# Optimization experiments

Hardware: AMD Instinct MI355X
Metric: run time of the kernel (lower is better)

## Reference

```python
import jax, jax.numpy as jnp
import numpy as np

NUM_NODES = 100000
NUM_EDGES = 50000
N_INC = 1000000  # incidence pairs (node, hyperedge)
IN_DIM = 128
EDGE_DIM = 128
NODE_DIM = 128


def _glorot(key, fan_in, fan_out):
    lim = float(np.sqrt(6.0 / (fan_in + fan_out)))
    return jax.random.uniform(key, (fan_in, fan_out), jnp.float32, -lim, lim)


def _prelu(x, a):
    return jnp.where(x >= 0, x, a * x)


def setup_inputs() -> dict:
    key = jax.random.key(0)
    ks = jax.random.split(key, 7)
    x = jax.random.normal(ks[0], (NUM_NODES, IN_DIM), jnp.float32)
    node_idx = jax.random.randint(ks[1], (N_INC,), 0, NUM_NODES, jnp.int32)
    edge_idx = jax.random.randint(ks[2], (N_INC,), 0, NUM_EDGES, jnp.int32)
    hyperedge_index = jnp.stack([node_idx, edge_idx])  # [2, N_INC]
    return dict(
        x=x,
        hyperedge_index=hyperedge_index,
        W_n2e_0=_glorot(ks[3], IN_DIM, EDGE_DIM),
        W_e2n_0=_glorot(ks[4], EDGE_DIM, NODE_DIM),
        bias_0=jnp.zeros((NODE_DIM,), jnp.float32),
        W_n2e_1=_glorot(ks[5], NODE_DIM, EDGE_DIM),
        W_e2n_1=_glorot(ks[6], EDGE_DIM, NODE_DIM),
        bias_1=jnp.zeros((NODE_DIM,), jnp.float32),
        alpha=jnp.float32(0.25),  # shared nn.PReLU() parameter
        num_nodes=NUM_NODES,
        num_edges=NUM_EDGES,
    )


def _conv(x, node_idx, edge_idx, Dn_inv, De_inv, W_n2e, W_e2n, b, alpha,
          num_nodes, num_edges):
    # node -> hyperedge: row-normalized scatter-add (norm = De^{-1} per target edge)
    xe = x @ W_n2e                                              # [N, E_dim]
    msg_e = xe[node_idx] * De_inv[edge_idx][:, None]            # [N_INC, E_dim]
    e = jax.ops.segment_sum(msg_e, edge_idx, num_segments=num_edges)
    e = _prelu(e, alpha)
    # hyperedge -> node: norm = Dn^{-1} per target node
    xn = e @ W_e2n                                              # [M, D]
    msg_n = xn[edge_idx] * Dn_inv[node_idx][:, None]            # [N_INC, D]
    n = jax.ops.segment_sum(msg_n, node_idx, num_segments=num_nodes) + b
    return n, e


def reference(x, hyperedge_index, W_n2e_0, W_e2n_0, bias_0, W_n2e_1, W_e2n_1,
              bias_1, alpha, num_nodes, num_edges):
    node_idx = hyperedge_index[0]
    edge_idx = hyperedge_index[1]
    ones = jnp.ones((node_idx.shape[0],), jnp.float32)
    Dn = jax.ops.segment_sum(ones, node_idx, num_segments=num_nodes)
    De = jax.ops.segment_sum(ones, edge_idx, num_segments=num_edges)
    Dn_inv = jnp.where(Dn > 0, 1.0 / jnp.where(Dn > 0, Dn, 1.0), 0.0)
    De_inv = jnp.where(De > 0, 1.0 / jnp.where(De > 0, De, 1.0), 0.0)

    n, e = _conv(x, node_idx, edge_idx, Dn_inv, De_inv,
                 W_n2e_0, W_e2n_0, bias_0, alpha, num_nodes, num_edges)
    n = _prelu(n, alpha)  # encoder-level activation between layers
    n, e = _conv(n, node_idx, edge_idx, Dn_inv, De_inv,
                 W_n2e_1, W_e2n_1, bias_1, alpha, num_nodes, num_edges)
    n = _prelu(n, alpha)
    return n, e
```

## Files before the change

### kernel.cpp

```cpp
#include <hip/hip_runtime.h>
#include <stdint.h>

#define NN 100000
#define NE 50000
#define NBLK 256
#define NBK 196
#define ESH 8
#define NSH 9

using bf16x8 = __attribute__((ext_vector_type(8))) short;
using f32x4  = __attribute__((ext_vector_type(4))) float;

__device__ inline unsigned f2bf(float f) {
  union { float f; unsigned u; } x; x.f = f;
  unsigned u = x.u;
  return (u + 0x7FFFu + ((u >> 16) & 1u)) >> 16;
}
__device__ inline float bfbits2f(unsigned bits) {
  union { unsigned u; float f; } x; x.u = bits;
  return x.f;
}


__global__ __launch_bounds__(256) void hist_kernel(const int* __restrict__ nidx,
                                                   const int* __restrict__ eidx, int ni,
                                                   int* __restrict__ He, int* __restrict__ Hn) {
  __shared__ int he[NBK], hn[NBK];
  for (int t = threadIdx.x; t < NBK; t += 256) { he[t] = 0; hn[t] = 0; }
  __syncthreads();
  int chunk = (ni + NBLK - 1) / NBLK;
  int s = blockIdx.x * chunk, e = min(s + chunk, ni);
  for (int i = s + threadIdx.x; i < e; i += 256) {
    atomicAdd(&he[eidx[i] >> ESH], 1);
    atomicAdd(&hn[nidx[i] >> NSH], 1);
  }
  __syncthreads();
  for (int t = threadIdx.x; t < NBK; t += 256) {
    He[t * NBLK + blockIdx.x] = he[t];
    Hn[t * NBLK + blockIdx.x] = hn[t];
  }
}

__global__ __launch_bounds__(256) void scanH_kernel(int* __restrict__ He, int* __restrict__ Hn,
                                                    int* __restrict__ ebb, int* __restrict__ nbb,
                                                    int ni) {
  int* H = blockIdx.x ? Hn : He;
  int* bb = blockIdx.x ? nbb : ebb;
  __shared__ int tot[256];
  int t = threadIdx.x;
  int sum = 0;
  if (t < NBK)
    for (int b = 0; b < NBLK; b++) sum += H[t * NBLK + b];
  tot[t] = sum;
  __syncthreads();
  for (int o = 1; o < 256; o <<= 1) {
    int v = (t >= o) ? tot[t - o] : 0;
    __syncthreads();
    tot[t] += v;
    __syncthreads();
  }
  int base = (t > 0) ? tot[t - 1] : 0;
  if (t < NBK) {
    bb[t] = base;
    int run = base;
    for (int b = 0; b < NBLK; b++) {
      int old = H[t * NBLK + b];
      H[t * NBLK + b] = run;
      run += old;
    }
  }
  if (t == 0) bb[NBK] = ni;
}

__global__ __launch_bounds__(256) void scatter_kernel(const int* __restrict__ nidx,
                                                      const int* __restrict__ eidx, int ni,
                                                      const int* __restrict__ He,
                                                      const int* __restrict__ Hn,
                                                      unsigned* __restrict__ binE,
                                                      unsigned* __restrict__ binN) {
  __shared__ int ce[NBK], cn[NBK];
  for (int t = threadIdx.x; t < NBK; t += 256) {
    ce[t] = He[t * NBLK + blockIdx.x];
    cn[t] = Hn[t * NBLK + blockIdx.x];
  }
  __syncthreads();
  int chunk = (ni + NBLK - 1) / NBLK;
  int s = blockIdx.x * chunk, e = min(s + chunk, ni);
  for (int i = s + threadIdx.x; i < e; i += 256) {
    int nd = nidx[i], ed = eidx[i];
    int pe = atomicAdd(&ce[ed >> ESH], 1);
    binE[pe] = (unsigned)nd | ((unsigned)(ed & 255) << 17);
    int pn = atomicAdd(&cn[nd >> NSH], 1);
    binN[pn] = (unsigned)ed | ((unsigned)(nd & 511) << 16);
  }
}

__global__ __launch_bounds__(256) void finalize_kernel(const unsigned* __restrict__ binE,
                                                       const unsigned* __restrict__ binN,
                                                       const int* __restrict__ ebb,
                                                       const int* __restrict__ nbb,
                                                       int* __restrict__ eoff, int* __restrict__ noff,
                                                       float* __restrict__ einv, float* __restrict__ ninv,
                                                       int* __restrict__ edge_nodes,
                                                       int* __restrict__ node_edges, int ni) {
  __shared__ int cnt[512], excl[512], sc[256];
  bool isE = blockIdx.x < NBK;
  int b = isE ? blockIdx.x : blockIdx.x - NBK;
  const unsigned* bin = isE ? binE : binN;
  const int* bb = isE ? ebb : nbb;
  int* off = isE ? eoff : noff;
  float* inv = isE ? einv : ninv;
  int* out = isE ? edge_nodes : node_edges;
  int NT = isE ? NE : NN;
  int sh = isE ? ESH : NSH;
  int psh = isE ? 17 : 16;
  unsigned smask = (1u << psh) - 1u;
  int tbase = b << sh;
  int nt = min(1 << sh, NT - tbase);
  int t = threadIdx.x;
  cnt[t] = 0; cnt[t + 256] = 0;
  __syncthreads();
  int s = bb[b], e = bb[b + 1];
  for (int i = s + t; i < e; i += 256) atomicAdd(&cnt[bin[i] >> psh], 1);
  __syncthreads();
  int p = cnt[2 * t] + cnt[2 * t + 1];
  sc[t] = p;
  __syncthreads();
  for (int o = 1; o < 256; o <<= 1) {
    int v = (t >= o) ? sc[t - o] : 0;
    __syncthreads();
    sc[t] += v;
    __syncthreads();
  }
  int pb = (t > 0) ? sc[t - 1] : 0;
  excl[2 * t] = pb;
  excl[2 * t + 1] = pb + cnt[2 * t];
  __syncthreads();
  for (int lt = t; lt < nt; lt += 256) {
    off[tbase + lt] = s + excl[lt];
    int c = cnt[lt];
    inv[tbase + lt] = (c > 0) ? 1.0f / (float)c : 0.0f;
  }
  if (b == NBK - 1 && t == 0) off[NT] = ni;
  __syncthreads();
  cnt[t] = 0; cnt[t + 256] = 0;
  __syncthreads();
  for (int i = s + t; i < e; i += 256) {
    unsigned it = bin[i];
    int lt = it >> psh;
    int pos = s + excl[lt] + atomicAdd(&cnt[lt], 1);
    out[pos] = (int)(it & smask);
  }
}

__global__ void packw_kernel(const float* __restrict__ w0, const float* __restrict__ w1,
                             const float* __restrict__ w2, const float* __restrict__ w3,
                             short* __restrict__ wp) {
  int gid = blockIdx.x * blockDim.x + threadIdx.x;
  if (gid >= 4 * 16384) return;
  int w = gid >> 14, r = gid & 16383;
  int j = r & 7, lane = (r >> 3) & 63, kk = (r >> 9) & 3, ct = (r >> 11) & 7;
  int k = kk * 32 + (lane >> 4) * 8 + j;
  int c = ct * 16 + (lane & 15);
  const float* W = (w == 0) ? w0 : (w == 1) ? w1 : (w == 2) ? w2 : w3;
  wp[gid] = (short)f2bf(W[k * 128 + c]);
}

__global__ __launch_bounds__(256) void cvtrow_kernel(const float* __restrict__ x,
                                                     uint4* __restrict__ xb) {
  size_t q = (size_t)blockIdx.x * 256 + threadIdx.x;
  const float4* xf = (const float4*)x;
  float4 lo = xf[q * 2], hi = xf[q * 2 + 1];
  uint4 o;
  o.x = (f2bf(lo.x) & 0xffffu) | (f2bf(lo.y) << 16);
  o.y = (f2bf(lo.z) & 0xffffu) | (f2bf(lo.w) << 16);
  o.z = (f2bf(hi.x) & 0xffffu) | (f2bf(hi.y) << 16);
  o.w = (f2bf(hi.z) & 0xffffu) | (f2bf(hi.w) << 16);
  xb[q] = o;
}

template <bool PRELU, bool OBF>
__global__ __launch_bounds__(256) void gather_kernel(const uint4* __restrict__ src,
                                                     void* __restrict__ dst,
                                                     const int* __restrict__ off,
                                                     const int* __restrict__ ids,
                                                     const float* __restrict__ inv,
                                                     const float* __restrict__ bias,
                                                     const float* __restrict__ alpha_p, int T) {
  int tgt = blockIdx.x * 16 + (threadIdx.x >> 4);
  if (tgt >= T) return;
  int c = threadIdx.x & 15;
  int s = off[tgt], e = off[tgt + 1];
  float r[8] = {0, 0, 0, 0, 0, 0, 0, 0};
  int i = s;
  for (; i + 8 <= e; i += 8) {
    int idv[8];
#pragma unroll
    for (int u = 0; u < 8; u++) idv[u] = ids[i + u];
    uint4 v[8];
#pragma unroll
    for (int u = 0; u < 8; u++) v[u] = src[(size_t)idv[u] * 16 + c];
#pragma unroll
    for (int u = 0; u < 8; u++) {
      r[0] += bfbits2f(v[u].x << 16); r[1] += bfbits2f(v[u].x & 0xffff0000u);
      r[2] += bfbits2f(v[u].y << 16); r[3] += bfbits2f(v[u].y & 0xffff0000u);
      r[4] += bfbits2f(v[u].z << 16); r[5] += bfbits2f(v[u].z & 0xffff0000u);
      r[6] += bfbits2f(v[u].w << 16); r[7] += bfbits2f(v[u].w & 0xffff0000u);
    }
  }
  for (; i < e; i++) {
    uint4 v = src[(size_t)ids[i] * 16 + c];
    r[0] += bfbits2f(v.x << 16); r[1] += bfbits2f(v.x & 0xffff0000u);
    r[2] += bfbits2f(v.y << 16); r[3] += bfbits2f(v.y & 0xffff0000u);
    r[4] += bfbits2f(v.z << 16); r[5] += bfbits2f(v.z & 0xffff0000u);
    r[6] += bfbits2f(v.w << 16); r[7] += bfbits2f(v.w & 0xffff0000u);
  }
  float scv = inv[tgt];
  float al = PRELU ? *alpha_p : 0.f;
  float b[8] = {0, 0, 0, 0, 0, 0, 0, 0};
  if (bias) {
    float4 b0 = ((const float4*)bias)[c * 2];
    float4 b1 = ((const float4*)bias)[c * 2 + 1];
    b[0] = b0.x; b[1] = b0.y; b[2] = b0.z; b[3] = b0.w;
    b[4] = b1.x; b[5] = b1.y; b[6] = b1.z; b[7] = b1.w;
  }
#pragma unroll
  for (int j = 0; j < 8; j++) {
    float v = r[j] * scv + b[j];
    if constexpr (PRELU) v = (v >= 0.f) ? v : al * v;
    r[j] = v;
  }
  if constexpr (OBF) {
    uint4 o;
    o.x = (f2bf(r[0]) & 0xffffu) | (f2bf(r[1]) << 16);
    o.y = (f2bf(r[2]) & 0xffffu) | (f2bf(r[3]) << 16);
    o.z = (f2bf(r[4]) & 0xffffu) | (f2bf(r[5]) << 16);
    o.w = (f2bf(r[6]) & 0xffffu) | (f2bf(r[7]) << 16);
    ((uint4*)dst)[(size_t)tgt * 16 + c] = o;
  } else {
    float4 o0; o0.x = r[0]; o0.y = r[1]; o0.z = r[2]; o0.w = r[3];
    float4 o1; o1.x = r[4]; o1.y = r[5]; o1.z = r[6]; o1.w = r[7];
    ((float4*)dst)[(size_t)tgt * 32 + c * 2] = o0;
    ((float4*)dst)[(size_t)tgt * 32 + c * 2 + 1] = o1;
  }
}

template <bool WEF32>
__global__ __launch_bounds__(256) void gemm12_kernel(const short* __restrict__ A,
                                                     const short* __restrict__ wpA,
                                                     const short* __restrict__ wpB,
                                                     const float* __restrict__ alpha_p,
                                                     short* __restrict__ xn,
                                                     float* __restrict__ eoutf, int M) {
  __shared__ short tile[64][136];
  int wave = threadIdx.x >> 6;
  int lane = threadIdx.x & 63;
  int kg = lane >> 4;
  int rloc = lane & 15;
  int base = blockIdx.x * 64;
  int row = base + wave * 16 + rloc;
  float al = *alpha_p;

  bf16x8 a[4];
  if (row < M) {
    const short* arow = A + (size_t)row * 128 + kg * 8;
#pragma unroll
    for (int kk = 0; kk < 4; kk++) a[kk] = *(const bf16x8*)(arow + kk * 32);
  } else {
#pragma unroll
    for (int kk = 0; kk < 4; kk++) a[kk] = bf16x8{0, 0, 0, 0, 0, 0, 0, 0};
  }

#pragma unroll
  for (int ct = 0; ct < 8; ct++) {
    f32x4 acc = {0.f, 0.f, 0.f, 0.f};
#pragma unroll
    for (int kk = 0; kk < 4; kk++) {
      bf16x8 bfr = *(const bf16x8*)(wpA + ((size_t)(ct * 4 + kk) * 64 + lane) * 8);
      acc = __builtin_amdgcn_mfma_f32_16x16x32_bf16(a[kk], bfr, acc, 0, 0, 0);
    }
    int col = ct * 16 + rloc;
#pragma unroll
    for (int j = 0; j < 4; j++) {
      float v = acc[j];
      v = (v >= 0.f) ? v : al * v;
      int lrow = wave * 16 + kg * 4 + j;
      int grow = base + lrow;
      if (WEF32 && grow < M) eoutf[(size_t)grow * 128 + col] = v;
      tile[lrow][col] = (short)f2bf(v);
    }
  }

  bf16x8 a2[4];
#pragma unroll
  for (int kk = 0; kk < 4; kk++)
    a2[kk] = *(const bf16x8*)&tile[wave * 16 + rloc][kg * 8 + kk * 32];
#pragma unroll
  for (int ct = 0; ct < 8; ct++) {
    f32x4 acc = {0.f, 0.f, 0.f, 0.f};
#pragma unroll
    for (int kk = 0; kk < 4; kk++) {
      bf16x8 bfr = *(const bf16x8*)(wpB + ((size_t)(ct * 4 + kk) * 64 + lane) * 8);
      acc = __builtin_amdgcn_mfma_f32_16x16x32_bf16(a2[kk], bfr, acc, 0, 0, 0);
    }
    int col = ct * 16 + rloc;
#pragma unroll
    for (int j = 0; j < 4; j++) {
      int grow = base + wave * 16 + kg * 4 + j;
      if (grow < M) xn[(size_t)grow * 128 + col] = (short)f2bf(acc[j]);
    }
  }
}

extern "C" void kernel_launch(void* const* d_in, const int* in_sizes, int n_in,
                              void* d_out, int out_size, void* d_ws, size_t ws_size,
                              hipStream_t stream) {
  const float* x = (const float*)d_in[0];
  const int* nidx = (const int*)d_in[1];
  int NI = in_sizes[1] / 2;
  const int* eidx = nidx + NI;
  const float* W0 = (const float*)d_in[2];
  const float* W1 = (const float*)d_in[3];
  const float* b0 = (const float*)d_in[4];
  const float* W2 = (const float*)d_in[5];
  const float* W3 = (const float*)d_in[6];
  const float* b1 = (const float*)d_in[7];
  const float* alpha = (const float*)d_in[8];

  char* ws = (char*)d_ws;
  size_t o = 0;
  auto alloc = [&](size_t bytes) { void* p = ws + o; o += (bytes + 255) & ~255ull; return p; };
  int* He = (int*)alloc((size_t)NBK * NBLK * 4);
  int* Hn = (int*)alloc((size_t)NBK * NBLK * 4);
  int* ebb = (int*)alloc((NBK + 1) * 4);
  int* nbb = (int*)alloc((NBK + 1) * 4);
  int* eoff = (int*)alloc((size_t)(NE + 1) * 4);
  int* noff = (int*)alloc((size_t)(NN + 1) * 4);
  float* einv = (float*)alloc((size_t)NE * 4);
  float* ninv = (float*)alloc((size_t)NN * 4);
  int* edge_nodes = (int*)alloc((size_t)NI * 4);
  int* node_edges = (int*)alloc((size_t)NI * 4);
  short* wp = (short*)alloc((size_t)4 * 16384 * 2);
  char* arena = (char*)alloc((size_t)NN * 128 * 2 + (size_t)NE * 128 * 2 * 2);
  unsigned* binE = (unsigned*)arena;
  unsigned* binN = (unsigned*)(arena + (size_t)NI * 4);
  short* xb = (short*)arena;
  short* Ge = (short*)(arena + (size_t)NN * 128 * 2);
  short* xn = (short*)(arena + (size_t)NN * 128 * 2 + (size_t)NE * 128 * 2);

  float* outN = (float*)d_out;
  float* outE = outN + (size_t)NN * 128;

  hist_kernel<<<NBLK, 256, 0, stream>>>(nidx, eidx, NI, He, Hn);
  scanH_kernel<<<2, 256, 0, stream>>>(He, Hn, ebb, nbb, NI);
  scatter_kernel<<<NBLK, 256, 0, stream>>>(nidx, eidx, NI, He, Hn, binE, binN);
  finalize_kernel<<<2 * NBK, 256, 0, stream>>>(binE, binN, ebb, nbb, eoff, noff,
                                               einv, ninv, edge_nodes, node_edges, NI);
  packw_kernel<<<256, 256, 0, stream>>>(W0, W1, W2, W3, wp);
  cvtrow_kernel<<<NN * 128 / 8 / 256, 256, 0, stream>>>(x, (uint4*)xb);

  int gfE = (NE + 63) / 64;
  int ggE = NE / 16;
  int ggN = (NN + 15) / 16;

  gather_kernel<false, true><<<ggE, 256, 0, stream>>>((const uint4*)xb, Ge, eoff, edge_nodes,
                                                      einv, nullptr, alpha, NE);
  gemm12_kernel<false><<<gfE, 256, 0, stream>>>(Ge, wp + 0 * 16384, wp + 1 * 16384,
                                                alpha, xn, nullptr, NE);
  short* n1 = xb;
  gather_kernel<true, true><<<ggN, 256, 0, stream>>>((const uint4*)xn, n1, noff, node_edges,
                                                     ninv, b0, alpha, NN);
  gather_kernel<false, true><<<ggE, 256, 0, stream>>>((const uint4*)n1, Ge, eoff, edge_nodes,
                                                      einv, nullptr, alpha, NE);
  gemm12_kernel<true><<<gfE, 256, 0, stream>>>(Ge, wp + 2 * 16384, wp + 3 * 16384,
                                               alpha, xn, outE, NE);
  gather_kernel<true, false><<<ggN, 256, 0, stream>>>((const uint4*)xn, outN, noff, node_edges,
                                                      ninv, b1, alpha, NN);
}
```

Baseline: 288.2 us.

## Split feature columns into XCC-local chunks with work-stealing gathers

Feature matrices are stored column-chunked: eight 16-column slices, each laid out contiguously over all rows. A persistent gather kernel reads the XCC id and starts on the chunk matching its die, so each die's L2 only caches one eighth of the source table. Work is handed out through per-chunk atomic counters, with stealing from other chunks once a die's own chunk is done. The cvt, gemm and output paths are changed to match the chunked layout. This costs extra shuffle reductions, atomics and a memset, and it relies on the hardware XCC-to-chunk mapping.

```diff
diff --git a/kernel.cpp b/kernel.cpp
--- a/kernel.cpp
+++ b/kernel.cpp
@@ -166,82 +166,116 @@
   wp[gid] = (short)f2bf(W[k * 128 + c]);
 }
 
-__global__ __launch_bounds__(256) void cvtrow_kernel(const float* __restrict__ x,
-                                                     uint4* __restrict__ xb) {
-  size_t q = (size_t)blockIdx.x * 256 + threadIdx.x;
-  const float4* xf = (const float4*)x;
-  float4 lo = xf[q * 2], hi = xf[q * 2 + 1];
-  uint4 o;
-  o.x = (f2bf(lo.x) & 0xffffu) | (f2bf(lo.y) << 16);
-  o.y = (f2bf(lo.z) & 0xffffu) | (f2bf(lo.w) << 16);
-  o.z = (f2bf(hi.x) & 0xffffu) | (f2bf(hi.y) << 16);
-  o.w = (f2bf(hi.z) & 0xffffu) | (f2bf(hi.w) << 16);
-  xb[q] = o;
-}
-
-template <bool PRELU, bool OBF>
-__global__ __launch_bounds__(256) void gather_kernel(const uint4* __restrict__ src,
-                                                     void* __restrict__ dst,
-                                                     const int* __restrict__ off,
-                                                     const int* __restrict__ ids,
-                                                     const float* __restrict__ inv,
-                                                     const float* __restrict__ bias,
-                                                     const float* __restrict__ alpha_p, int T) {
-  int tgt = blockIdx.x * 16 + (threadIdx.x >> 4);
-  if (tgt >= T) return;
-  int c = threadIdx.x & 15;
-  int s = off[tgt], e = off[tgt + 1];
-  float r[8] = {0, 0, 0, 0, 0, 0, 0, 0};
-  int i = s;
-  for (; i + 8 <= e; i += 8) {
-    int idv[8];
-#pragma unroll
-    for (int u = 0; u < 8; u++) idv[u] = ids[i + u];
-    uint4 v[8];
-#pragma unroll
-    for (int u = 0; u < 8; u++) v[u] = src[(size_t)idv[u] * 16 + c];
-#pragma unroll
-    for (int u = 0; u < 8; u++) {
-      r[0] += bfbits2f(v[u].x << 16); r[1] += bfbits2f(v[u].x & 0xffff0000u);
-      r[2] += bfbits2f(v[u].y << 16); r[3] += bfbits2f(v[u].y & 0xffff0000u);
-      r[4] += bfbits2f(v[u].z << 16); r[5] += bfbits2f(v[u].z & 0xffff0000u);
-      r[6] += bfbits2f(v[u].w << 16); r[7] += bfbits2f(v[u].w & 0xffff0000u);
-    }
-  }
-  for (; i < e; i++) {
-    uint4 v = src[(size_t)ids[i] * 16 + c];
-    r[0] += bfbits2f(v.x << 16); r[1] += bfbits2f(v.x & 0xffff0000u);
-    r[2] += bfbits2f(v.y << 16); r[3] += bfbits2f(v.y & 0xffff0000u);
-    r[4] += bfbits2f(v.z << 16); r[5] += bfbits2f(v.z & 0xffff0000u);
-    r[6] += bfbits2f(v.w << 16); r[7] += bfbits2f(v.w & 0xffff0000u);
-  }
-  float scv = inv[tgt];
+__global__ __launch_bounds__(256) void cvt_kernel(const float* __restrict__ x,
+                                                  uint4* __restrict__ xb) {
+  __shared__ unsigned lds[128 * 65];
+  int t = threadIdx.x;
+  int rows0 = blockIdx.x * 128;
+#pragma unroll
+  for (int it = 0; it < 16; it++) {
+    int q = t + it * 256;
+    int row = q >> 5, f4 = q & 31;
+    if (rows0 + row < NN) {
+      float4 v = ((const float4*)x)[(size_t)(rows0 + row) * 32 + f4];
+      lds[row * 65 + f4 * 2]     = (f2bf(v.x) & 0xffffu) | (f2bf(v.y) << 16);
+      lds[row * 65 + f4 * 2 + 1] = (f2bf(v.z) & 0xffffu) | (f2bf(v.w) << 16);
+    }
+  }
+  __syncthreads();
+#pragma unroll
+  for (int it = 0; it < 8; it++) {
+    int q = t + it * 256;
+    int c = q >> 8, rem = q & 255, row = rem >> 1, h = rem & 1;
+    if (rows0 + row < NN) {
+      unsigned* p = &lds[row * 65 + c * 8 + h * 4];
+      uint4 o; o.x = p[0]; o.y = p[1]; o.z = p[2]; o.w = p[3];
+      xb[((size_t)c * NN + rows0 + row) * 2 + h] = o;
+    }
+  }
+}
+
+template <bool PRELU, int OUT>
+__global__ __launch_bounds__(256) void wgather_kernel(const uint4* __restrict__ src,
+                                                      void* __restrict__ dst,
+                                                      const int* __restrict__ off,
+                                                      const int* __restrict__ ids,
+                                                      const float* __restrict__ inv,
+                                                      const float* __restrict__ bias,
+                                                      const float* __restrict__ alpha_p,
+                                                      int T, int Rsrc,
+                                                      int* __restrict__ cnt) {
+  unsigned xcc;
+  asm volatile("s_getreg_b32 %0, hwreg(HW_REG_XCC_ID)" : "=s"(xcc));
+  int myc = (int)(xcc & 7u);
+  int lane = threadIdx.x & 63;
+  int tg4 = lane >> 4;
+  int l = lane & 15;
+  int slot = l >> 1, h = l & 1;
   float al = PRELU ? *alpha_p : 0.f;
-  float b[8] = {0, 0, 0, 0, 0, 0, 0, 0};
-  if (bias) {
-    float4 b0 = ((const float4*)bias)[c * 2];
-    float4 b1 = ((const float4*)bias)[c * 2 + 1];
-    b[0] = b0.x; b[1] = b0.y; b[2] = b0.z; b[3] = b0.w;
-    b[4] = b1.x; b[5] = b1.y; b[6] = b1.z; b[7] = b1.w;
-  }
-#pragma unroll
-  for (int j = 0; j < 8; j++) {
-    float v = r[j] * scv + b[j];
-    if constexpr (PRELU) v = (v >= 0.f) ? v : al * v;
-    r[j] = v;
-  }
-  if constexpr (OBF) {
-    uint4 o;
-    o.x = (f2bf(r[0]) & 0xffffu) | (f2bf(r[1]) << 16);
-    o.y = (f2bf(r[2]) & 0xffffu) | (f2bf(r[3]) << 16);
-    o.z = (f2bf(r[4]) & 0xffffu) | (f2bf(r[5]) << 16);
-    o.w = (f2bf(r[6]) & 0xffffu) | (f2bf(r[7]) << 16);
-    ((uint4*)dst)[(size_t)tgt * 16 + c] = o;
-  } else {
-    float4 o0; o0.x = r[0]; o0.y = r[1]; o0.z = r[2]; o0.w = r[3];
-    float4 o1; o1.x = r[4]; o1.y = r[5]; o1.z = r[6]; o1.w = r[7];
-    ((float4*)dst)[(size_t)tgt * 32 + c * 2] = o0;
-    ((float4*)dst)[(size_t)tgt * 32 + c * 2 + 1] = o1;
+  int nb = (T + 15) >> 4;
+
+  for (int stp = 0; stp < 8; stp++) {
+    int c = (myc + stp) & 7;
+    if (stp > 0) {
+      int cur = __hip_atomic_load(&cnt[c * 64], __ATOMIC_RELAXED, __HIP_MEMORY_SCOPE_AGENT);
+      if (cur >= nb) continue;
+    }
+    const uint4* base = src + (size_t)c * Rsrc * 2;
+    float bv[8] = {0, 0, 0, 0, 0, 0, 0, 0};
+    if (bias) {
+      float4 b0 = ((const float4*)bias)[c * 4 + h * 2];
+      float4 b1 = ((const float4*)bias)[c * 4 + h * 2 + 1];
+      bv[0] = b0.x; bv[1] = b0.y; bv[2] = b0.z; bv[3] = b0.w;
+      bv[4] = b1.x; bv[5] = b1.y; bv[6] = b1.z; bv[7] = b1.w;
+    }
+    for (;;) {
+      int tk = 0;
+      if (lane == 0) tk = atomicAdd(&cnt[c * 64], 1);
+      tk = __builtin_amdgcn_readfirstlane(tk);
+      if (tk >= nb) break;
+#pragma unroll
+      for (int pass = 0; pass < 4; pass++) {
+        int tgt = tk * 16 + pass * 4 + tg4;
+        if (tgt >= T) continue;
+        int s = off[tgt], e = off[tgt + 1];
+        float r[8] = {0, 0, 0, 0, 0, 0, 0, 0};
+        for (int i = s + slot; i < e; i += 8) {
+          int id = ids[i];
+          uint4 v = base[(size_t)id * 2 + h];
+          r[0] += bfbits2f(v.x << 16); r[1] += bfbits2f(v.x & 0xffff0000u);
+          r[2] += bfbits2f(v.y << 16); r[3] += bfbits2f(v.y & 0xffff0000u);
+          r[4] += bfbits2f(v.z << 16); r[5] += bfbits2f(v.z & 0xffff0000u);
+          r[6] += bfbits2f(v.w << 16); r[7] += bfbits2f(v.w & 0xffff0000u);
+        }
+#pragma unroll
+        for (int m = 2; m <= 8; m <<= 1) {
+#pragma unroll
+          for (int j = 0; j < 8; j++) r[j] += __shfl_xor(r[j], m);
+        }
+        if (slot == 0) {
+          float scv = inv[tgt];
+#pragma unroll
+          for (int j = 0; j < 8; j++) {
+            float v = r[j] * scv + bv[j];
+            if constexpr (PRELU) v = (v >= 0.f) ? v : al * v;
+            r[j] = v;
+          }
+          if constexpr (OUT == 0) {
+            uint4 o;
+            o.x = (f2bf(r[0]) & 0xffffu) | (f2bf(r[1]) << 16);
+            o.y = (f2bf(r[2]) & 0xffffu) | (f2bf(r[3]) << 16);
+            o.z = (f2bf(r[4]) & 0xffffu) | (f2bf(r[5]) << 16);
+            o.w = (f2bf(r[6]) & 0xffffu) | (f2bf(r[7]) << 16);
+            ((uint4*)dst)[((size_t)c * T + tgt) * 2 + h] = o;
+          } else {
+            float4 o0; o0.x = r[0]; o0.y = r[1]; o0.z = r[2]; o0.w = r[3];
+            float4 o1; o1.x = r[4]; o1.y = r[5]; o1.z = r[6]; o1.w = r[7];
+            ((float4*)dst)[(size_t)tgt * 32 + c * 4 + h * 2] = o0;
+            ((float4*)dst)[(size_t)tgt * 32 + c * 4 + h * 2 + 1] = o1;
+          }
+        }
+      }
+    }
   }
 }
 
@@ -263,9 +297,14 @@
 
   bf16x8 a[4];
   if (row < M) {
-    const short* arow = A + (size_t)row * 128 + kg * 8;
-#pragma unroll
-    for (int kk = 0; kk < 4; kk++) a[kk] = *(const bf16x8*)(arow + kk * 32);
+    const uint4* A4 = (const uint4*)A;
+#pragma unroll
+    for (int kk = 0; kk < 4; kk++) {
+      int c = kk * 2 + (kg >> 1);
+      uint4 v = A4[((size_t)c * M + row) * 2 + (kg & 1)];
+      union { uint4 u; bf16x8 b; } cv; cv.u = v;
+      a[kk] = cv.b;
+    }
   } else {
 #pragma unroll
     for (int kk = 0; kk < 4; kk++) a[kk] = bf16x8{0, 0, 0, 0, 0, 0, 0, 0};
@@ -303,11 +342,10 @@
       bf16x8 bfr = *(const bf16x8*)(wpB + ((size_t)(ct * 4 + kk) * 64 + lane) * 8);
       acc = __builtin_amdgcn_mfma_f32_16x16x32_bf16(a2[kk], bfr, acc, 0, 0, 0);
     }
-    int col = ct * 16 + rloc;
 #pragma unroll
     for (int j = 0; j < 4; j++) {
       int grow = base + wave * 16 + kg * 4 + j;
-      if (grow < M) xn[(size_t)grow * 128 + col] = (short)f2bf(acc[j]);
+      if (grow < M) xn[((size_t)ct * M + grow) * 16 + rloc] = (short)f2bf(acc[j]);
     }
   }
 }
@@ -341,39 +379,40 @@
   int* edge_nodes = (int*)alloc((size_t)NI * 4);
   int* node_edges = (int*)alloc((size_t)NI * 4);
   short* wp = (short*)alloc((size_t)4 * 16384 * 2);
+  int* cnt = (int*)alloc(4 * 512 * 4);
   char* arena = (char*)alloc((size_t)NN * 128 * 2 + (size_t)NE * 128 * 2 * 2);
   unsigned* binE = (unsigned*)arena;
   unsigned* binN = (unsigned*)(arena + (size_t)NI * 4);
-  short* xb = (short*)arena;
-  short* Ge = (short*)(arena + (size_t)NN * 128 * 2);
-  short* xn = (short*)(arena + (size_t)NN * 128 * 2 + (size_t)NE * 128 * 2);
+  short* xb  = (short*)arena;
+  short* Geb = (short*)(arena + (size_t)NN * 128 * 2);
+  short* xnb = (short*)(arena + (size_t)NN * 128 * 2 + (size_t)NE * 128 * 2);
 
   float* outN = (float*)d_out;
   float* outE = outN + (size_t)NN * 128;
 
+  hipMemsetAsync(cnt, 0, 4 * 512 * 4, stream);
   hist_kernel<<<NBLK, 256, 0, stream>>>(nidx, eidx, NI, He, Hn);
   scanH_kernel<<<2, 256, 0, stream>>>(He, Hn, ebb, nbb, NI);
   scatter_kernel<<<NBLK, 256, 0, stream>>>(nidx, eidx, NI, He, Hn, binE, binN);
   finalize_kernel<<<2 * NBK, 256, 0, stream>>>(binE, binN, ebb, nbb, eoff, noff,
                                                einv, ninv, edge_nodes, node_edges, NI);
   packw_kernel<<<256, 256, 0, stream>>>(W0, W1, W2, W3, wp);
-  cvtrow_kernel<<<NN * 128 / 8 / 256, 256, 0, stream>>>(x, (uint4*)xb);
+  cvt_kernel<<<(NN + 127) / 128, 256, 0, stream>>>(x, (uint4*)xb);
 
   int gfE = (NE + 63) / 64;
-  int ggE = NE / 16;
-  int ggN = (NN + 15) / 16;
-
-  gather_kernel<false, true><<<ggE, 256, 0, stream>>>((const uint4*)xb, Ge, eoff, edge_nodes,
-                                                      einv, nullptr, alpha, NE);
-  gemm12_kernel<false><<<gfE, 256, 0, stream>>>(Ge, wp + 0 * 16384, wp + 1 * 16384,
-                                                alpha, xn, nullptr, NE);
-  short* n1 = xb;
-  gather_kernel<true, true><<<ggN, 256, 0, stream>>>((const uint4*)xn, n1, noff, node_edges,
-                                                     ninv, b0, alpha, NN);
-  gather_kernel<false, true><<<ggE, 256, 0, stream>>>((const uint4*)n1, Ge, eoff, edge_nodes,
-                                                      einv, nullptr, alpha, NE);
-  gemm12_kernel<true><<<gfE, 256, 0, stream>>>(Ge, wp + 2 * 16384, wp + 3 * 16384,
-                                               alpha, xn, outE, NE);
-  gather_kernel<true, false><<<ggN, 256, 0, stream>>>((const uint4*)xn, outN, noff, node_edges,
-                                                      ninv, b1, alpha, NN);
-}
+  const int WG = 2048;
+
+  wgather_kernel<false, 0><<<WG, 256, 0, stream>>>((const uint4*)xb, Geb, eoff, edge_nodes,
+                                                   einv, nullptr, alpha, NE, NN, cnt + 0);
+  gemm12_kernel<false><<<gfE, 256, 0, stream>>>(Geb, wp + 0 * 16384, wp + 1 * 16384,
+                                                alpha, xnb, nullptr, NE);
+  short* n1b = xb;
+  wgather_kernel<true, 0><<<WG, 256, 0, stream>>>((const uint4*)xnb, n1b, noff, node_edges,
+                                                  ninv, b0, alpha, NN, NE, cnt + 512);
+  wgather_kernel<false, 0><<<WG, 256, 0, stream>>>((const uint4*)n1b, Geb, eoff, edge_nodes,
+                                                   einv, nullptr, alpha, NE, NN, cnt + 1024);
+  gemm12_kernel<true><<<gfE, 256, 0, stream>>>(Geb, wp + 2 * 16384, wp + 3 * 16384,
+                                               alpha, xnb, outE, NE);
+  wgather_kernel<true, 1><<<WG, 256, 0, stream>>>((const uint4*)xnb, outN, noff, node_edges,
+                                                  ninv, b1, alpha, NN, NE, cnt + 1536);
+}
```

New measurement: 861.1 us. 199% more time.
